# Kernel tuning notes

Hardware: AMD Instinct MI355X
Metric: run time of the kernel (lower is better)

## Reference

```python
import jax, jax.numpy as jnp
import numpy as np

N = 8192      # points
K = 16        # nsample neighbors
CIN = 64      # in_plane
C = 256       # out_plane (== mid_planes)
S = 8         # share_planes
EPS = 1e-5


def _bn(x, g, b, axes):
    # BatchNorm1d (training-mode batch stats, biased var), channel = last dim
    m = x.mean(axes, keepdims=True)
    v = x.var(axes, keepdims=True)
    return (x - m) / jnp.sqrt(v + EPS) * g + b


def _knn(p, k):
    # brute-force KNN over a single batch (o = [N]); indices include self
    sq = jnp.sum(p * p, axis=1)
    d2 = sq[:, None] + sq[None, :] - 2.0 * (p @ p.T)   # [N, N]
    idx = jax.lax.top_k(-d2, k)[1]                      # [N, K]
    return jax.lax.stop_gradient(idx)


def setup_inputs() -> dict:
    key = jax.random.key(0)
    ks = jax.random.split(key, 16)
    W = lambda i, shp, s=0.05: jax.random.normal(ks[i], shp, jnp.float32) * s
    one = lambda d: jnp.ones((d,), jnp.float32)
    zero = lambda d: jnp.zeros((d,), jnp.float32)
    return {
        "p": jax.random.normal(ks[0], (N, 3), jnp.float32),
        "x": jax.random.normal(ks[1], (N, CIN), jnp.float32),
        "o": jnp.array([N], dtype=jnp.int32),
        # PointAggregation (stride=1): Linear(no bias) + BN
        "W_pa": W(2, (CIN, C)), "g_pa": one(C), "b_pa": zero(C),
        # SelfFusion.linear1 (no bias) + bn1
        "W1": W(3, (C, C)), "g1": one(C), "b1": zero(C),
        # SelfFusionLayer q/k/v
        "Wq": W(4, (C, C)), "bq": zero(C),
        "Wk": W(5, (C, C)), "bk": zero(C),
        "Wv": W(6, (C, C)), "bv": zero(C),
        # linear_p: Linear(3,3)+BN(3)+ReLU+Linear(3,C)
        "Wp1": W(7, (3, 3), 0.3), "bp1": zero(3), "gp": one(3), "bp": zero(3),
        "Wp2": W(8, (3, C), 0.3), "bp2": zero(C),
        # linear_w: BN(C)+ReLU+Linear(C,C//S)+BN(C//S)+ReLU+Linear(C//S,C//S)
        "gw1": one(C), "bw1": zero(C),
        "Ww1": W(9, (C, C // S)), "bww1": zero(C // S),
        "gw2": one(C // S), "bw2": zero(C // S),
        "Ww2": W(10, (C // S, C // S), 0.2), "bww2": zero(C // S),
        # bn2, linear3 (no bias) + bn3
        "g2": one(C), "b2": zero(C),
        "W3": W(11, (C, C)), "g3": one(C), "b3": zero(C),
    }


def reference(p, x, o, W_pa, g_pa, b_pa, W1, g1, b1, Wq, bq, Wk, bk, Wv, bv,
              Wp1, bp1, gp, bp, Wp2, bp2, gw1, bw1, Ww1, bww1, gw2, bw2,
              Ww2, bww2, g2, b2, W3, g3, b3):
    relu = jax.nn.relu
    # --- PointAggregation (stride=1) ---
    h = relu(_bn(x @ W_pa, g_pa, b_pa, (0,)))          # [N, C]
    # --- SelfFusion block ---
    identity = h
    h = relu(_bn(h @ W1, g1, b1, (0,)))                # [N, C]
    # SelfFusionLayer
    xq = h @ Wq + bq                                   # [N, C]
    xk = h @ Wk + bk
    xv = h @ Wv + bv
    idx = _knn(p, K)                                   # [N, K]
    rel = p[idx] - p[:, None, :]                       # [N, K, 3] relative coords
    xk_g = xk[idx]                                     # [N, K, C]
    xv_g = xv[idx]                                     # [N, K, C]
    # linear_p: Linear(3,3) -> BN(3) -> ReLU -> Linear(3,C)
    p_r = rel @ Wp1 + bp1
    p_r = relu(_bn(p_r, gp, bp, (0, 1)))
    p_r = p_r @ Wp2 + bp2                              # [N, K, C]
    # mid_planes == out_planes so view(...).sum(2) is identity
    w = xk_g - xq[:, None, :] + p_r                    # [N, K, C]
    # linear_w: BN -> ReLU -> Linear -> BN -> ReLU -> Linear
    w = relu(_bn(w, gw1, bw1, (0, 1)))
    w = w @ Ww1 + bww1                                 # [N, K, C//S]
    w = relu(_bn(w, gw2, bw2, (0, 1)))
    w = w @ Ww2 + bww2                                 # [N, K, C//S]
    w = jax.nn.softmax(w, axis=1)                      # softmax over neighbors
    y = ((xv_g + p_r).reshape(N, K, S, C // S) * w[:, :, None, :]).sum(1)
    y = y.reshape(N, C)
    # back in SelfFusion
    y = relu(_bn(y, g2, b2, (0,)))
    y = _bn(y @ W3, g3, b3, (0,))
    x2 = relu(y + identity)
    return (p, x2, o)
```

## Files before the change

### kernel.cpp

```cpp
#include <hip/hip_runtime.h>
#include <hip/hip_bf16.h>

#define INV_N  (1.0f/8192.0f)
#define INV_NK (1.0f/131072.0f)

typedef __attribute__((ext_vector_type(8))) short bf16x8;
typedef __attribute__((ext_vector_type(4))) float f32x4;
typedef unsigned short u16;

__device__ __forceinline__ u16 f2b(float f) {
  unsigned u = __float_as_uint(f);
  return (u16)((u + 0x7FFFu + ((u >> 16) & 1u)) >> 16);
}
__device__ __forceinline__ float b2f(u16 u) {
  return __uint_as_float(((unsigned)u) << 16);
}

__device__ __forceinline__ float bn_ap(float v, const float* st, int C, int ch,
                                       float inv, float g, float b) {
  float m = st[ch] * inv;
  float var = st[C + ch] * inv - m * m;
  return (v - m) * rsqrtf(var + 1e-5f) * g + b;
}

__launch_bounds__(256)
__global__ void prep_k(const float* __restrict__ p, const int* __restrict__ o,
                       const float* __restrict__ Ww1,
                       float4* __restrict__ pp, u16* __restrict__ Ww1t,
                       float* __restrict__ st, float* __restrict__ out) {
  int b = blockIdx.x, t = threadIdx.x;
  int e = b*256 + t;
  if (b < 16) st[b*256 + t] = 0.f;
  if (e < 24576) out[e] = p[e];
  if (e == 0) out[24576 + 2097152] = (float)o[0];
  if (e < 8192) {
    float x = p[e*3+0], y = p[e*3+1], z = p[e*3+2];
    pp[e] = make_float4(x, y, z, (x*x + y*y) + z*z);
  }
  if (b >= 88) {
    int q = (b - 88)*1024 + t*4;
#pragma unroll
    for (int ii = 0; ii < 4; ++ii) {
      int e2 = q + ii;
      int k = e2 >> 5, n = e2 & 31;
      Ww1t[n*256 + k] = f2b(Ww1[e2]);
    }
  }
}

template<int ROWS, int SPLIT>
__launch_bounds__(256)
__global__ void red_k(const float* __restrict__ part, float* __restrict__ outp,
                      int width) {
  int ncg = width >> 6;
  int cg = blockIdx.x % ncg, sp = blockIdx.x / ncg;
  int lane = threadIdx.x & 63, chunk = threadIdx.x >> 6;
  int c = cg*64 + lane;
  constexpr int R  = ROWS / SPLIT;
  constexpr int RC = R / 4;
  float s = 0.f;
  int i0 = sp*R + chunk*RC;
#pragma unroll 4
  for (int i = i0; i < i0 + RC; ++i) s += part[(size_t)i*width + c];
  __shared__ float red[4][64];
  red[chunk][lane] = s;
  __syncthreads();
  if (threadIdx.x < 64) {
    float v = red[0][lane] + red[1][lane] + red[2][lane] + red[3][lane];
    if (SPLIT == 1) outp[c] = v;
    else atomicAdd(&outp[c], v);
  }
}

__device__ __forceinline__ void knn_dev(char* smem, const float4* __restrict__ pp,
                                        int* __restrict__ idxo, int kb) {
  float4* buf = (float4*)smem;
  int t = threadIdx.x;
  int wave = t >> 6, lane = t & 63;
  int q = kb*4 + wave;
  float4 qv = pp[q];
  const float BIG = __uint_as_float(0x7F7FFFFFu);
  float d[3];
#pragma unroll
  for (int s = 0; s < 3; ++s) d[s] = BIG;
  for (int ch = 0; ch < 8; ++ch) {
#pragma unroll
    for (int s = 0; s < 4; ++s)
      buf[s*256 + t] = pp[ch*1024 + s*256 + t];
    __syncthreads();
#pragma unroll 4
    for (int it = 0; it < 16; ++it) {
      int jl = it*64 + lane;
      float4 c = buf[jl];
      int j = ch*1024 + jl;
      float dot = qv.x*c.x + (qv.y*c.y + qv.z*c.z);
      float d2 = __fmaf_rn(-2.0f, dot, qv.w + c.w);
      float pk = __uint_as_float((__float_as_uint(d2) & 0xFFFFE000u) | (unsigned)j);
      d[2] = fminf(fmaxf(d[1], pk), d[2]);
      d[1] = fminf(fmaxf(d[0], pk), d[1]);
      d[0] = fminf(d[0], pk);
    }
    __syncthreads();
  }
  for (int r = 0; r < 16; ++r) {
    float bd = d[0];
#pragma unroll
    for (int m = 1; m < 64; m <<= 1)
      bd = fminf(bd, __shfl_xor(bd, m));
    if (lane == 0) idxo[q*16 + r] = (int)(__float_as_uint(bd) & 0x1FFFu);
    if (d[0] == bd) { d[0] = d[1]; d[1] = d[2]; d[2] = BIG; }
  }
}

template<typename TA, typename TO, bool BNA, bool STATS>
__device__ __forceinline__ void mfgemm_dev(char* smem,
    const TA* __restrict__ A, const float* __restrict__ st,
    const float* __restrict__ g, const float* __restrict__ bb, float inv_cnt,
    const float* __restrict__ W, TO* __restrict__ out,
    float* __restrict__ stout, int KA, int NOUT, int bm, int bn_) {
  short (*As)[72] = (short(*)[72])smem;
  short (*Bt)[72] = (short(*)[72])(smem + 9216);
  float* lscl = (float*)(smem + 18432);
  float* lsft = (float*)(smem + 19456);
  int t = threadIdx.x;
  int m0 = bm * 64, n0 = bn_ * 64;
  if (BNA) {
    for (int e = t; e < KA; e += 256) {
      float m = st[e] * inv_cnt;
      float var = st[KA + e] * inv_cnt - m*m;
      float sc = rsqrtf(var + 1e-5f) * g[e];
      lscl[e] = sc; lsft[e] = bb[e] - m*sc;
    }
    __syncthreads();
  }
  const f32x4 zero = {0.f, 0.f, 0.f, 0.f};
  f32x4 acc[2][2] = {{zero, zero}, {zero, zero}};
  int wv = t >> 6, l = t & 63;
  int wm = wv & 1, wn = wv >> 1;
  int lr = l & 15, lk = (l >> 4) * 8;
  int ra = t >> 4, qa = t & 15;
  int bn = t & 63, bkc = t >> 6;
  for (int k0 = 0; k0 < KA; k0 += 64) {
#pragma unroll
    for (int rp = 0; rp < 4; ++rp) {
      int r = rp*16 + ra;
      float vv[4];
      if constexpr (sizeof(TA) == 4) {
        float4 av = *(const float4*)((const float*)A + (size_t)(m0 + r)*KA + k0 + qa*4);
        vv[0] = av.x; vv[1] = av.y; vv[2] = av.z; vv[3] = av.w;
      } else {
        short4 av = *(const short4*)((const u16*)A + (size_t)(m0 + r)*KA + k0 + qa*4);
#pragma unroll
        for (int jj = 0; jj < 4; ++jj) vv[jj] = b2f(((u16*)&av)[jj]);
      }
      short4 s;
#pragma unroll
      for (int jj = 0; jj < 4; ++jj) {
        float v = vv[jj];
        if (BNA) { int ch = k0 + qa*4 + jj; v = fmaxf(fmaf(v, lscl[ch], lsft[ch]), 0.f); }
        ((u16*)&s)[jj] = f2b(v);
      }
      *(short4*)&As[r][qa*4] = s;
    }
    {
      float v[16];
#pragma unroll
      for (int j2 = 0; j2 < 16; ++j2)
        v[j2] = W[(size_t)(k0 + bkc*16 + j2)*NOUT + n0 + bn];
      bf16x8 w0, w1v;
#pragma unroll
      for (int j2 = 0; j2 < 8; ++j2) {
        w0[j2]  = (short)f2b(v[j2]);
        w1v[j2] = (short)f2b(v[8 + j2]);
      }
      *(bf16x8*)&Bt[bn][bkc*16]     = w0;
      *(bf16x8*)&Bt[bn][bkc*16 + 8] = w1v;
    }
    __syncthreads();
#pragma unroll
    for (int fk = 0; fk < 2; ++fk) {
      bf16x8 a0 = *(const bf16x8*)&As[wm*32 +      lr][fk*32 + lk];
      bf16x8 a1 = *(const bf16x8*)&As[wm*32 + 16 + lr][fk*32 + lk];
      bf16x8 b0 = *(const bf16x8*)&Bt[wn*32 +      lr][fk*32 + lk];
      bf16x8 b1 = *(const bf16x8*)&Bt[wn*32 + 16 + lr][fk*32 + lk];
      acc[0][0] = __builtin_amdgcn_mfma_f32_16x16x32_bf16(a0, b0, acc[0][0], 0, 0, 0);
      acc[0][1] = __builtin_amdgcn_mfma_f32_16x16x32_bf16(a0, b1, acc[0][1], 0, 0, 0);
      acc[1][0] = __builtin_amdgcn_mfma_f32_16x16x32_bf16(a1, b0, acc[1][0], 0, 0, 0);
      acc[1][1] = __builtin_amdgcn_mfma_f32_16x16x32_bf16(a1, b1, acc[1][1], 0, 0, 0);
    }
    __syncthreads();
  }
#pragma unroll
  for (int fn = 0; fn < 2; ++fn) {
    int col = n0 + wn*32 + fn*16 + lr;
    float s1 = 0.f, s2 = 0.f;
#pragma unroll
    for (int fm = 0; fm < 2; ++fm) {
#pragma unroll
      for (int r = 0; r < 4; ++r) {
        int row = m0 + wm*32 + fm*16 + (l >> 4)*4 + r;
        float v = acc[fm][fn][r];
        if constexpr (sizeof(TO) == 4) out[(size_t)row*NOUT + col] = v;
        else                           out[(size_t)row*NOUT + col] = f2b(v);
        if (STATS) { s1 += v; s2 += v*v; }
      }
    }
    if (STATS) {
      s1 += __shfl_xor(s1, 16); s1 += __shfl_xor(s1, 32);
      s2 += __shfl_xor(s2, 16); s2 += __shfl_xor(s2, 32);
      if (l < 16) {
        atomicAdd(&stout[col], s1);
        atomicAdd(&stout[NOUT + col], s2);
      }
    }
  }
}

__device__ __forceinline__ void comp_pr1(const float* p, int i, int j,
                                         const float* Wp1, const float* bp1,
                                         float pr1[3]) {
  float rx = p[j*3+0] - p[i*3+0];
  float ry = p[j*3+1] - p[i*3+1];
  float rz = p[j*3+2] - p[i*3+2];
#pragma unroll
  for (int c = 0; c < 3; ++c)
    pr1[c] = rx*Wp1[c] + ry*Wp1[3+c] + rz*Wp1[6+c] + bp1[c];
}

__device__ __forceinline__ void comp_prv(const float* p, int i, int j,
                                         const float* Wp1, const float* bp1,
                                         const float* gp, const float* bpp,
                                         const float* sp, float o3[3]) {
  float pr1[3];
  comp_pr1(p, i, j, Wp1, bp1, pr1);
#pragma unroll
  for (int c = 0; c < 3; ++c)
    o3[c] = fmaxf(bn_ap(pr1[c], sp, 3, c, INV_NK, gp[c], bpp[c]), 0.0f);
}

__device__ __forceinline__ void prstats_dev(char* smem,
    const float* __restrict__ p, const int* __restrict__ idx,
    const float* Wp1, const float* bp1, float* __restrict__ sp, int pb) {
  float s[3] = {0,0,0}, s2[3] = {0,0,0};
  for (int it = 0; it < 4; ++it) {
    int e = pb*1024 + it*256 + threadIdx.x;
    int i = e >> 4;
    int j = idx[e] & 8191;
    float pr1[3];
    comp_pr1(p, i, j, Wp1, bp1, pr1);
#pragma unroll
    for (int c = 0; c < 3; ++c) { s[c] += pr1[c]; s2[c] += pr1[c]*pr1[c]; }
  }
#pragma unroll
  for (int m = 1; m < 64; m <<= 1) {
#pragma unroll
    for (int c = 0; c < 3; ++c) {
      s[c]  += __shfl_xor(s[c],  m);
      s2[c] += __shfl_xor(s2[c], m);
    }
  }
  float (*red)[6] = (float(*)[6])smem;
  int wv = threadIdx.x >> 6, lane = threadIdx.x & 63;
  if (lane == 0) {
#pragma unroll
    for (int c = 0; c < 3; ++c) { red[wv][c] = s[c]; red[wv][3+c] = s2[c]; }
  }
  __syncthreads();
  if (threadIdx.x < 6) {
    float v = red[0][threadIdx.x] + red[1][threadIdx.x] +
              red[2][threadIdx.x] + red[3][threadIdx.x];
    atomicAdd(&sp[threadIdx.x], v);
  }
}

__launch_bounds__(256)
__global__ void gemmknn_k(const float* __restrict__ x, const float* __restrict__ W_pa,
                          u16* __restrict__ t0, float* __restrict__ st0,
                          const float4* __restrict__ pp, int* __restrict__ idxo) {
  extern __shared__ char smem[];
  int b = blockIdx.x;
  if (b < 512)
    mfgemm_dev<float, u16, false, true>(smem, x, nullptr, nullptr, nullptr, 0.f,
                                        W_pa, t0, st0, 64, 256, b & 127, b >> 7);
  else
    knn_dev(smem, pp, idxo, b - 512);
}

__launch_bounds__(256)
__global__ void gemmpr_k(const u16* __restrict__ t0, const float* __restrict__ st0,
                         const float* __restrict__ g_pa, const float* __restrict__ b_pa,
                         const float* __restrict__ W1, u16* __restrict__ t1,
                         float* __restrict__ st1,
                         const float* __restrict__ p, const int* __restrict__ idx,
                         const float* __restrict__ Wp1, const float* __restrict__ bp1,
                         float* __restrict__ sp) {
  extern __shared__ char smem[];
  int b = blockIdx.x;
  if (b < 512)
    mfgemm_dev<u16, u16, true, true>(smem, t0, st0, g_pa, b_pa, INV_N,
                                     W1, t1, st1, 256, 256, b & 127, b >> 7);
  else
    prstats_dev(smem, p, idx, Wp1, bp1, sp, b - 512);
}

template<typename TA, typename TO, bool BNA, bool STATS>
__launch_bounds__(256)
__global__ void mfgemm_k(const TA* __restrict__ A, const float* __restrict__ st,
                         const float* __restrict__ g, const float* __restrict__ bb,
                         float inv_cnt,
                         const float* __restrict__ W, TO* __restrict__ out,
                         float* __restrict__ stout, int KA, int NOUT) {
  extern __shared__ char smem[];
  mfgemm_dev<TA, TO, BNA, STATS>(smem, A, st, g, bb, inv_cnt, W, out, stout,
                                 KA, NOUT, blockIdx.x, blockIdx.y);
}

__launch_bounds__(256)
__global__ void qkv_k(const u16* __restrict__ t1, const float* __restrict__ st,
                      const float* __restrict__ g1, const float* __restrict__ b1,
                      const float* __restrict__ Wq, const float* __restrict__ bq,
                      const float* __restrict__ Wk, const float* __restrict__ bk,
                      const float* __restrict__ Wv, const float* __restrict__ bv,
                      u16* __restrict__ xq, u16* __restrict__ xk, u16* __restrict__ xv) {
  __shared__ short As[64][72];
  __shared__ short Bt[3][64][72];
  __shared__ float lscl[256], lsft[256];
  int t = threadIdx.x;
  int m0 = blockIdx.x * 64, n0 = blockIdx.y * 64;
  {
    int e = t;
    float m = st[e] * INV_N;
    float var = st[256 + e] * INV_N - m*m;
    float sc = rsqrtf(var + 1e-5f) * g1[e];
    lscl[e] = sc; lsft[e] = b1[e] - m*sc;
  }
  __syncthreads();
  const f32x4 zero = {0.f, 0.f, 0.f, 0.f};
  f32x4 acc[3][2][2];
#pragma unroll
  for (int w = 0; w < 3; ++w)
#pragma unroll
    for (int i = 0; i < 2; ++i)
#pragma unroll
      for (int j = 0; j < 2; ++j) acc[w][i][j] = zero;
  int wv = t >> 6, l = t & 63;
  int wm = wv & 1, wn = wv >> 1;
  int lr = l & 15, lk = (l >> 4) * 8;
  int ra = t >> 4, qa = t & 15;
  int bn = t & 63, bkc = t >> 6;
  const float* Ws[3] = {Wq, Wk, Wv};
  for (int k0 = 0; k0 < 256; k0 += 64) {
#pragma unroll
    for (int rp = 0; rp < 4; ++rp) {
      int r = rp*16 + ra;
      short4 av = *(const short4*)(t1 + (size_t)(m0 + r)*256 + k0 + qa*4);
      short4 s;
#pragma unroll
      for (int jj = 0; jj < 4; ++jj) {
        int ch = k0 + qa*4 + jj;
        float v = fmaxf(fmaf(b2f(((u16*)&av)[jj]), lscl[ch], lsft[ch]), 0.f);
        ((u16*)&s)[jj] = f2b(v);
      }
      *(short4*)&As[r][qa*4] = s;
    }
#pragma unroll
    for (int w = 0; w < 3; ++w) {
      float v[16];
#pragma unroll
      for (int j2 = 0; j2 < 16; ++j2)
        v[j2] = Ws[w][(size_t)(k0 + bkc*16 + j2)*256 + n0 + bn];
      bf16x8 w0, w1v;
#pragma unroll
      for (int j2 = 0; j2 < 8; ++j2) {
        w0[j2]  = (short)f2b(v[j2]);
        w1v[j2] = (short)f2b(v[8 + j2]);
      }
      *(bf16x8*)&Bt[w][bn][bkc*16]     = w0;
      *(bf16x8*)&Bt[w][bn][bkc*16 + 8] = w1v;
    }
    __syncthreads();
#pragma unroll
    for (int fk = 0; fk < 2; ++fk) {
      bf16x8 a0 = *(const bf16x8*)&As[wm*32 +      lr][fk*32 + lk];
      bf16x8 a1 = *(const bf16x8*)&As[wm*32 + 16 + lr][fk*32 + lk];
#pragma unroll
      for (int w = 0; w < 3; ++w) {
        bf16x8 b0 = *(const bf16x8*)&Bt[w][wn*32 +      lr][fk*32 + lk];
        bf16x8 b1 = *(const bf16x8*)&Bt[w][wn*32 + 16 + lr][fk*32 + lk];
        acc[w][0][0] = __builtin_amdgcn_mfma_f32_16x16x32_bf16(a0, b0, acc[w][0][0], 0, 0, 0);
        acc[w][0][1] = __builtin_amdgcn_mfma_f32_16x16x32_bf16(a0, b1, acc[w][0][1], 0, 0, 0);
        acc[w][1][0] = __builtin_amdgcn_mfma_f32_16x16x32_bf16(a1, b0, acc[w][1][0], 0, 0, 0);
        acc[w][1][1] = __builtin_amdgcn_mfma_f32_16x16x32_bf16(a1, b1, acc[w][1][1], 0, 0, 0);
      }
    }
    __syncthreads();
  }
  u16* outs[3] = {xq, xk, xv};
  const float* bs[3] = {bq, bk, bv};
#pragma unroll
  for (int w = 0; w < 3; ++w) {
#pragma unroll
    for (int fn = 0; fn < 2; ++fn) {
      int col = n0 + wn*32 + fn*16 + lr;
      float bvv = bs[w][col];
#pragma unroll
      for (int fm = 0; fm < 2; ++fm) {
#pragma unroll
        for (int r = 0; r < 4; ++r) {
          int row = m0 + wm*32 + fm*16 + (l >> 4)*4 + r;
          outs[w][(size_t)row*256 + col] = f2b(acc[w][fm][fn][r] + bvv);
        }
      }
    }
  }
}

__launch_bounds__(256)
__global__ void stats256_k(const u16* __restrict__ X, float* __restrict__ psy) {
  int c = threadIdx.x;
  int r0 = blockIdx.x * 32;
  float s1 = 0.f, s2 = 0.f;
  for (int r = 0; r < 32; ++r) {
    float v = b2f(X[(size_t)(r0 + r)*256 + c]);
    s1 += v; s2 += v*v;
  }
  psy[(size_t)blockIdx.x*512 + c]       = s1;
  psy[(size_t)blockIdx.x*512 + 256 + c] = s2;
}

__launch_bounds__(256)
__global__ void wstats_k(const u16* __restrict__ xk, const u16* __restrict__ xq,
                         const float* __restrict__ p, const int* __restrict__ idx,
                         const float* Wp1, const float* bp1, const float* gp, const float* bpp,
                         const float* sp, const float* __restrict__ Wp2, const float* bp2,
                         float* __restrict__ pws) {
  __shared__ float prv[8][16][4];
  __shared__ int   jidx[8][16];
  int base = blockIdx.x * 8;
  int t = threadIdx.x;
  if (t < 128) {
    int pt = t >> 4, k = t & 15;
    int j = idx[(base + pt)*16 + k] & 8191;
    jidx[pt][k] = j;
    float o3[3];
    comp_prv(p, base + pt, j, Wp1, bp1, gp, bpp, sp, o3);
    prv[pt][k][0] = o3[0]; prv[pt][k][1] = o3[1]; prv[pt][k][2] = o3[2];
  }
  __syncthreads();
  int c = t;
  float wp0 = Wp2[c], wp1v = Wp2[256+c], wp2v = Wp2[512+c];
  float bbv = bp2[c];
  float s1 = 0.f, s2 = 0.f;
  for (int pt = 0; pt < 8; ++pt) {
    int i = base + pt;
    float xqv = b2f(xq[(size_t)i*256 + c]);
    u16 kvals[16];
#pragma unroll
    for (int k = 0; k < 16; ++k)
      kvals[k] = xk[(size_t)jidx[pt][k]*256 + c];
#pragma unroll
    for (int k = 0; k < 16; ++k) {
      float pr = prv[pt][k][0]*wp0 + prv[pt][k][1]*wp1v + prv[pt][k][2]*wp2v + bbv;
      float wval = b2f(kvals[k]) - xqv + pr;
      s1 += wval; s2 += wval*wval;
    }
  }
  pws[(size_t)blockIdx.x*512 + c]       = s1;
  pws[(size_t)blockIdx.x*512 + 256 + c] = s2;
}

__launch_bounds__(256)
__global__ void w1gemm_k(const u16* __restrict__ xk, const u16* __restrict__ xq,
                         const float* __restrict__ p, const int* __restrict__ idx,
                         const float* Wp1, const float* bp1, const float* gp, const float* bpp,
                         const float* sp, const float* __restrict__ Wp2, const float* bp2,
                         const float* sw, const float* gw1, const float* bw1,
                         const u16* __restrict__ Ww1t, const float* bww1,
                         u16* __restrict__ w1, float* __restrict__ pw1) {
  __shared__ short sA[64][264];
  __shared__ float prv[64][3];
  __shared__ int   jrow[64];
  __shared__ float sred[256];
  int t = threadIdx.x;
  int base4 = blockIdx.x * 4;
  if (t < 64) {
    int grow = blockIdx.x*64 + t;
    int j = idx[grow] & 8191;
    jrow[t] = j;
    float o3[3];
    comp_prv(p, grow >> 4, j, Wp1, bp1, gp, bpp, sp, o3);
    prv[t][0] = o3[0]; prv[t][1] = o3[1]; prv[t][2] = o3[2];
  }
  __syncthreads();
  {
    int o = t & 31, rs = t >> 5;
    int ch0 = o*8;
    int jr[8];
#pragma unroll
    for (int ii = 0; ii < 8; ++ii) jr[ii] = jrow[ii*8 + rs];
    bf16x8 kvv[8], qvv[8];
#pragma unroll
    for (int ii = 0; ii < 8; ++ii) {
      int r = ii*8 + rs;
      kvv[ii] = *(const bf16x8*)(xk + (size_t)jr[ii]*256 + ch0);
      qvv[ii] = *(const bf16x8*)(xq + (size_t)(base4 + (r >> 4))*256 + ch0);
    }
    float sclv[8], sftv[8], w0v[8], w1vv[8], w2v[8], b2v[8];
#pragma unroll
    for (int h = 0; h < 2; ++h) {
      float4 swm = *(const float4*)(sw + ch0 + h*4);
      float4 sws = *(const float4*)(sw + 256 + ch0 + h*4);
      float4 g4  = *(const float4*)(gw1 + ch0 + h*4);
      float4 bb4 = *(const float4*)(bw1 + ch0 + h*4);
      float4 p0v = *(const float4*)(Wp2 + ch0 + h*4);
      float4 p1v = *(const float4*)(Wp2 + 256 + ch0 + h*4);
      float4 p2v = *(const float4*)(Wp2 + 512 + ch0 + h*4);
      float4 bp4 = *(const float4*)(bp2 + ch0 + h*4);
      float mv[4] = {swm.x, swm.y, swm.z, swm.w};
      float sv[4] = {sws.x, sws.y, sws.z, sws.w};
      float gv[4] = {g4.x, g4.y, g4.z, g4.w};
      float bv[4] = {bb4.x, bb4.y, bb4.z, bb4.w};
      float a0[4] = {p0v.x, p0v.y, p0v.z, p0v.w};
      float a1[4] = {p1v.x, p1v.y, p1v.z, p1v.w};
      float a2[4] = {p2v.x, p2v.y, p2v.z, p2v.w};
      float a3[4] = {bp4.x, bp4.y, bp4.z, bp4.w};
#pragma unroll
      for (int jj = 0; jj < 4; ++jj) {
        int e = h*4 + jj;
        float m = mv[jj]*INV_NK;
        float var = sv[jj]*INV_NK - m*m;
        float sc = rsqrtf(var + 1e-5f)*gv[jj];
        sclv[e] = sc; sftv[e] = bv[jj] - m*sc;
        w0v[e] = a0[jj]; w1vv[e] = a1[jj]; w2v[e] = a2[jj]; b2v[e] = a3[jj];
      }
    }
#pragma unroll
    for (int ii = 0; ii < 8; ++ii) {
      int r = ii*8 + rs;
      float p0 = prv[r][0], p1 = prv[r][1], p2 = prv[r][2];
      bf16x8 av;
#pragma unroll
      for (int e = 0; e < 8; ++e) {
        float v = b2f((u16)kvv[ii][e]) - b2f((u16)qvv[ii][e])
                + p0*w0v[e] + p1*w1vv[e] + p2*w2v[e] + b2v[e];
        v = fmaxf(fmaf(v, sclv[e], sftv[e]), 0.f);
        av[e] = (short)f2b(v);
      }
      *(bf16x8*)&sA[r][ch0] = av;
    }
  }
  __syncthreads();
  const f32x4 zero = {0.f,0.f,0.f,0.f};
  f32x4 acc[2] = {zero, zero};
  int wv = t >> 6, l = t & 63;
  int lr = l & 15, hi = l >> 4;
#pragma unroll
  for (int k0 = 0; k0 < 8; ++k0) {
    int kb = k0*32 + hi*8;
    bf16x8 a  = *(const bf16x8*)&sA[wv*16 + lr][kb];
    bf16x8 b0 = *(const bf16x8*)(Ww1t + (size_t)lr*256      + kb);
    bf16x8 b1 = *(const bf16x8*)(Ww1t + (size_t)(16+lr)*256 + kb);
    acc[0] = __builtin_amdgcn_mfma_f32_16x16x32_bf16(a, b0, acc[0], 0, 0, 0);
    acc[1] = __builtin_amdgcn_mfma_f32_16x16x32_bf16(a, b1, acc[1], 0, 0, 0);
  }
#pragma unroll
  for (int fn = 0; fn < 2; ++fn) {
    int col = fn*16 + lr;
    float bv = bww1[col];
    float s1 = 0.f, s2 = 0.f;
#pragma unroll
    for (int r = 0; r < 4; ++r) {
      int grow = blockIdx.x*64 + wv*16 + hi*4 + r;
      float v = acc[fn][r] + bv;
      w1[(size_t)grow*32 + col] = f2b(v);
      s1 += v; s2 += v*v;
    }
    s1 += __shfl_xor(s1, 16); s1 += __shfl_xor(s1, 32);
    s2 += __shfl_xor(s2, 16); s2 += __shfl_xor(s2, 32);
    if (l < 16) { sred[(wv*2+fn)*16 + lr] = s1; sred[128 + (wv*2+fn)*16 + lr] = s2; }
  }
  __syncthreads();
  if (t < 32) {
    float a = 0.f, b = 0.f;
#pragma unroll
    for (int w2 = 0; w2 < 4; ++w2) {
      a += sred[(w2*2 + (t >> 4))*16 + (t & 15)];
      b += sred[128 + (w2*2 + (t >> 4))*16 + (t & 15)];
    }
    pw1[(size_t)blockIdx.x*64 + t]      = a;
    pw1[(size_t)blockIdx.x*64 + 32 + t] = b;
  }
}

__launch_bounds__(256)
__global__ void aggr_k(const u16* __restrict__ w1, const float* sw1,
                       const float* gw2, const float* bw2,
                       const float* __restrict__ Ww2, const float* bww2,
                       const u16* __restrict__ xv,
                       const float* __restrict__ p, const int* __restrict__ idx,
                       const float* Wp1, const float* bp1, const float* gp, const float* bpp,
                       const float* sp, const float* __restrict__ Wp2, const float* bp2,
                       u16* __restrict__ y) {
  __shared__ float lw1[16][32];
  __shared__ float lW2[32][32];
  __shared__ float sw2[16][33];
  __shared__ float prv[16][4];
  __shared__ int   jidx[16];
  int i = blockIdx.x, t = threadIdx.x;
  for (int e = t; e < 1024; e += 256) lW2[e >> 5][e & 31] = Ww2[e];
  for (int e = t; e < 512; e += 256) {
    int c32 = e & 31;
    float v = b2f(w1[(size_t)i*512 + e]);
    v = fmaxf(bn_ap(v, sw1, 32, c32, INV_NK, gw2[c32], bw2[c32]), 0.0f);
    lw1[e >> 5][c32] = v;
  }
  if (t < 16) jidx[t] = idx[i*16 + t] & 8191;
  __syncthreads();
  if (t < 16) {
    float o3[3];
    comp_prv(p, i, jidx[t], Wp1, bp1, gp, bpp, sp, o3);
    prv[t][0] = o3[0]; prv[t][1] = o3[1]; prv[t][2] = o3[2];
  }
  for (int e = t; e < 512; e += 256) {
    int k = e >> 5, c32 = e & 31;
    float a = bww2[c32];
#pragma unroll
    for (int j = 0; j < 32; ++j) a += lw1[k][j] * lW2[j][c32];
    sw2[k][c32] = a;
  }
  __syncthreads();
  if (t < 32) {
    float mx = -3.0e38f;
#pragma unroll
    for (int k = 0; k < 16; ++k) mx = fmaxf(mx, sw2[k][t]);
    float s = 0.f;
#pragma unroll
    for (int k = 0; k < 16; ++k) { float e2 = expf(sw2[k][t] - mx); sw2[k][t] = e2; s += e2; }
    float r = 1.0f / s;
#pragma unroll
    for (int k = 0; k < 16; ++k) sw2[k][t] *= r;
  }
  __syncthreads();
  int c = t;
  float wp0 = Wp2[c], wp1v = Wp2[256+c], wp2v = Wp2[512+c];
  float bbv = bp2[c];
  int c32 = c & 31;
  float acc = 0.f;
#pragma unroll
  for (int k = 0; k < 16; ++k) {
    int j = jidx[k];
    float pr = prv[k][0]*wp0 + prv[k][1]*wp1v + prv[k][2]*wp2v + bbv;
    float xvv = b2f(xv[(size_t)j*256 + c]);
    acc += (xvv + pr) * sw2[k][c32];
  }
  y[(size_t)i*256 + c] = f2b(acc);
}

__launch_bounds__(256)
__global__ void final_k(const u16* __restrict__ t0, const float* s0,
                        const float* g0, const float* b0,
                        const u16* __restrict__ t3, const float* s3,
                        const float* g3, const float* b3,
                        float* __restrict__ out) {
  int i = blockIdx.x, c = threadIdx.x;
  size_t off = (size_t)i*256 + c;
  float h0 = fmaxf(bn_ap(b2f(t0[off]), s0, 256, c, INV_N, g0[c], b0[c]), 0.0f);
  float v3 = bn_ap(b2f(t3[off]), s3, 256, c, INV_N, g3[c], b3[c]);
  out[24576 + off] = fmaxf(v3 + h0, 0.0f);
}

extern "C" void kernel_launch(void* const* d_in, const int* in_sizes, int n_in,
                              void* d_out, int out_size, void* d_ws, size_t ws_size,
                              hipStream_t stream) {
  (void)in_sizes; (void)n_in; (void)out_size; (void)ws_size;
  const float* p    = (const float*)d_in[0];
  const float* x    = (const float*)d_in[1];
  const int*   o    = (const int*)  d_in[2];
  const float* W_pa = (const float*)d_in[3];
  const float* g_pa = (const float*)d_in[4];
  const float* b_pa = (const float*)d_in[5];
  const float* W1   = (const float*)d_in[6];
  const float* g1   = (const float*)d_in[7];
  const float* b1   = (const float*)d_in[8];
  const float* Wq   = (const float*)d_in[9];
  const float* bq   = (const float*)d_in[10];
  const float* Wk   = (const float*)d_in[11];
  const float* bk   = (const float*)d_in[12];
  const float* Wv   = (const float*)d_in[13];
  const float* bv   = (const float*)d_in[14];
  const float* Wp1  = (const float*)d_in[15];
  const float* bp1  = (const float*)d_in[16];
  const float* gp   = (const float*)d_in[17];
  const float* bpp  = (const float*)d_in[18];
  const float* Wp2  = (const float*)d_in[19];
  const float* bp2  = (const float*)d_in[20];
  const float* gw1  = (const float*)d_in[21];
  const float* bw1  = (const float*)d_in[22];
  const float* Ww1  = (const float*)d_in[23];
  const float* bww1 = (const float*)d_in[24];
  const float* gw2  = (const float*)d_in[25];
  const float* bw2  = (const float*)d_in[26];
  const float* Ww2  = (const float*)d_in[27];
  const float* bww2 = (const float*)d_in[28];
  const float* g2   = (const float*)d_in[29];
  const float* b2   = (const float*)d_in[30];
  const float* W3   = (const float*)d_in[31];
  const float* g3   = (const float*)d_in[32];
  const float* b3   = (const float*)d_in[33];

  char* ws = (char*)d_ws;
  u16*   t0  = (u16*)  (ws + 0);
  u16*   t1  = (u16*)  (ws + 4194304);
  u16*   xq  = (u16*)  (ws + 8388608);
  u16*   xk  = (u16*)  (ws + 12582912);
  u16*   xv  = (u16*)  (ws + 16777216);
  u16*   w1  = (u16*)  (ws + 20971520);
  int*   idx = (int*)  (ws + 29360128);
  float* st  = (float*)(ws + 29884416);
  u16*   Ww1t= (u16*)  (ws + 29900800);
  float* pw1 = (float*)(ws + 30408704);
  float* pws = (float*)(ws + 30932992);
  float* psy = (float*)(ws + 33030144);
  u16*   y   = t1;
  u16*   t3  = xq;
  float4* pp = (float4*)(ws + 20971520);

  prep_k<<<96, 256, 0, stream>>>(p, o, Ww1, pp, Ww1t, st, (float*)d_out);

  gemmknn_k<<<2560, 256, 20480, stream>>>(x, W_pa, t0, st + 0, pp, idx);

  gemmpr_k<<<640, 256, 20480, stream>>>(t0, st + 0, g_pa, b_pa, W1, t1, st + 512,
                                        p, idx, Wp1, bp1, st + 2624);

  qkv_k<<<dim3(128, 4), 256, 0, stream>>>(
      t1, st + 512, g1, b1, Wq, bq, Wk, bk, Wv, bv, xq, xk, xv);

  wstats_k<<<1024, 256, 0, stream>>>(xk, xq, p, idx, Wp1, bp1, gp, bpp,
                                     st + 2624, Wp2, bp2, pws);
  red_k<1024, 4><<<32, 256, 0, stream>>>(pws, st + 1024, 512);

  w1gemm_k<<<2048, 256, 0, stream>>>(xk, xq, p, idx, Wp1, bp1, gp, bpp,
                                     st + 2624, Wp2, bp2, st + 1024,
                                     gw1, bw1, Ww1t, bww1, w1, pw1);
  red_k<2048, 16><<<16, 256, 0, stream>>>(pw1, st + 2560, 64);

  aggr_k<<<8192, 256, 0, stream>>>(w1, st + 2560, gw2, bw2, Ww2, bww2, xv,
                                   p, idx, Wp1, bp1, gp, bpp, st + 2624,
                                   Wp2, bp2, y);
  stats256_k<<<256, 256, 0, stream>>>(y, psy);
  red_k<256, 2><<<16, 256, 0, stream>>>(psy, st + 1536, 512);

  mfgemm_k<u16, u16, true, true><<<dim3(128, 4), 256, 20480, stream>>>(
      y, st + 1536, g2, b2, INV_N, W3, t3, st + 2048, 256, 256);

  final_k<<<8192, 256, 0, stream>>>(t0, st + 0, g_pa, b_pa,
                                    t3, st + 2048, g3, b3, (float*)d_out);
}
```

Before: 187.2 us.

## Spread KNN blocks across the GEMM and QKV launches to overlap work

The KNN search used to share one launch with the first small GEMM. It is now split into two halves: one half runs alongside the second GEMM and the other alongside the QKV projection, each launched as extra blocks. The first GEMM becomes a standalone launch, and the pr-stats reduction moves into its own kernel after idx is complete. The aim is to balance the heterogeneous work across launches so the KNN fills idle compute units during the heavier GEMMs. In exchange it adds one kernel launch, and the QKV kernel now uses dynamic shared memory sized for its tiles (38912 B).

```diff
diff --git a/kernel.cpp b/kernel.cpp
--- a/kernel.cpp
+++ b/kernel.cpp
@@ -238,12 +238,12 @@
     o3[c] = fmaxf(bn_ap(pr1[c], sp, 3, c, INV_NK, gp[c], bpp[c]), 0.0f);
 }
 
-__device__ __forceinline__ void prstats_dev(char* smem,
-    const float* __restrict__ p, const int* __restrict__ idx,
-    const float* Wp1, const float* bp1, float* __restrict__ sp, int pb) {
+__launch_bounds__(256)
+__global__ void prstats_k(const float* __restrict__ p, const int* __restrict__ idx,
+                          const float* Wp1, const float* bp1, float* __restrict__ sp) {
   float s[3] = {0,0,0}, s2[3] = {0,0,0};
   for (int it = 0; it < 4; ++it) {
-    int e = pb*1024 + it*256 + threadIdx.x;
+    int e = blockIdx.x*1024 + it*256 + threadIdx.x;
     int i = e >> 4;
     int j = idx[e] & 8191;
     float pr1[3];
@@ -259,7 +259,7 @@
       s2[c] += __shfl_xor(s2[c], m);
     }
   }
-  float (*red)[6] = (float(*)[6])smem;
+  __shared__ float red[4][6];
   int wv = threadIdx.x >> 6, lane = threadIdx.x & 63;
   if (lane == 0) {
 #pragma unroll
@@ -273,34 +273,106 @@
   }
 }
 
-__launch_bounds__(256)
-__global__ void gemmknn_k(const float* __restrict__ x, const float* __restrict__ W_pa,
-                          u16* __restrict__ t0, float* __restrict__ st0,
-                          const float4* __restrict__ pp, int* __restrict__ idxo) {
-  extern __shared__ char smem[];
-  int b = blockIdx.x;
-  if (b < 512)
-    mfgemm_dev<float, u16, false, true>(smem, x, nullptr, nullptr, nullptr, 0.f,
-                                        W_pa, t0, st0, 64, 256, b & 127, b >> 7);
-  else
-    knn_dev(smem, pp, idxo, b - 512);
-}
-
-__launch_bounds__(256)
-__global__ void gemmpr_k(const u16* __restrict__ t0, const float* __restrict__ st0,
-                         const float* __restrict__ g_pa, const float* __restrict__ b_pa,
-                         const float* __restrict__ W1, u16* __restrict__ t1,
-                         float* __restrict__ st1,
-                         const float* __restrict__ p, const int* __restrict__ idx,
-                         const float* __restrict__ Wp1, const float* __restrict__ bp1,
-                         float* __restrict__ sp) {
-  extern __shared__ char smem[];
-  int b = blockIdx.x;
-  if (b < 512)
-    mfgemm_dev<u16, u16, true, true>(smem, t0, st0, g_pa, b_pa, INV_N,
-                                     W1, t1, st1, 256, 256, b & 127, b >> 7);
-  else
-    prstats_dev(smem, p, idx, Wp1, bp1, sp, b - 512);
+__device__ __forceinline__ void qkv_dev(char* smem,
+    const u16* __restrict__ t1, const float* __restrict__ st,
+    const float* __restrict__ g1, const float* __restrict__ b1,
+    const float* __restrict__ Wq, const float* __restrict__ bq,
+    const float* __restrict__ Wk, const float* __restrict__ bk,
+    const float* __restrict__ Wv, const float* __restrict__ bv,
+    u16* __restrict__ xq, u16* __restrict__ xk, u16* __restrict__ xv_,
+    int bm, int bn_) {
+  short (*As)[72] = (short(*)[72])smem;
+  short (*Bt)[64][72] = (short(*)[64][72])(smem + 9216);
+  float* lscl = (float*)(smem + 36864);
+  float* lsft = (float*)(smem + 37888);
+  int t = threadIdx.x;
+  int m0 = bm * 64, n0 = bn_ * 64;
+  {
+    int e = t;
+    float m = st[e] * INV_N;
+    float var = st[256 + e] * INV_N - m*m;
+    float sc = rsqrtf(var + 1e-5f) * g1[e];
+    lscl[e] = sc; lsft[e] = b1[e] - m*sc;
+  }
+  __syncthreads();
+  const f32x4 zero = {0.f, 0.f, 0.f, 0.f};
+  f32x4 acc[3][2][2];
+#pragma unroll
+  for (int w = 0; w < 3; ++w)
+#pragma unroll
+    for (int i = 0; i < 2; ++i)
+#pragma unroll
+      for (int j = 0; j < 2; ++j) acc[w][i][j] = zero;
+  int wv = t >> 6, l = t & 63;
+  int wm = wv & 1, wn = wv >> 1;
+  int lr = l & 15, lk = (l >> 4) * 8;
+  int ra = t >> 4, qa = t & 15;
+  int bn = t & 63, bkc = t >> 6;
+  const float* Ws[3] = {Wq, Wk, Wv};
+  for (int k0 = 0; k0 < 256; k0 += 64) {
+#pragma unroll
+    for (int rp = 0; rp < 4; ++rp) {
+      int r = rp*16 + ra;
+      short4 av = *(const short4*)(t1 + (size_t)(m0 + r)*256 + k0 + qa*4);
+      short4 s;
+#pragma unroll
+      for (int jj = 0; jj < 4; ++jj) {
+        int ch = k0 + qa*4 + jj;
+        float v = fmaxf(fmaf(b2f(((u16*)&av)[jj]), lscl[ch], lsft[ch]), 0.f);
+        ((u16*)&s)[jj] = f2b(v);
+      }
+      *(short4*)&As[r][qa*4] = s;
+    }
+#pragma unroll
+    for (int w = 0; w < 3; ++w) {
+      float v[16];
+#pragma unroll
+      for (int j2 = 0; j2 < 16; ++j2)
+        v[j2] = Ws[w][(size_t)(k0 + bkc*16 + j2)*256 + n0 + bn];
+      bf16x8 w0, w1v;
+#pragma unroll
+      for (int j2 = 0; j2 < 8; ++j2) {
+        w0[j2]  = (short)f2b(v[j2]);
+        w1v[j2] = (short)f2b(v[8 + j2]);
+      }
+      *(bf16x8*)&Bt[w][bn][bkc*16]     = w0;
+      *(bf16x8*)&Bt[w][bn][bkc*16 + 8] = w1v;
+    }
+    __syncthreads();
+#pragma unroll
+    for (int fk = 0; fk < 2; ++fk) {
+      bf16x8 a0 = *(const bf16x8*)&As[wm*32 +      lr][fk*32 + lk];
+      bf16x8 a1 = *(const bf16x8*)&As[wm*32 + 16 + lr][fk*32 + lk];
+#pragma unroll
+      for (int w = 0; w < 3; ++w) {
+        bf16x8 b0 = *(const bf16x8*)&Bt[w][wn*32 +      lr][fk*32 + lk];
+        bf16x8 b1 = *(const bf16x8*)&Bt[w][wn*32 + 16 + lr][fk*32 + lk];
+        acc[w][0][0] = __builtin_amdgcn_mfma_f32_16x16x32_bf16(a0, b0, acc[w][0][0], 0, 0, 0);
+        acc[w][0][1] = __builtin_amdgcn_mfma_f32_16x16x32_bf16(a0, b1, acc[w][0][1], 0, 0, 0);
+        acc[w][1][0] = __builtin_amdgcn_mfma_f32_16x16x32_bf16(a1, b0, acc[w][1][0], 0, 0, 0);
+        acc[w][1][1] = __builtin_amdgcn_mfma_f32_16x16x32_bf16(a1, b1, acc[w][1][1], 0, 0, 0);
+      }
+    }
+    __syncthreads();
+  }
+  u16* outs[3] = {xq, xk, xv_};
+  const float* bs[3] = {bq, bk, bv};
+#pragma unroll
+  for (int w = 0; w < 3; ++w) {
+#pragma unroll
+    for (int fn = 0; fn < 2; ++fn) {
+      int col = n0 + wn*32 + fn*16 + lr;
+      float bvv = bs[w][col];
+#pragma unroll
+      for (int fm = 0; fm < 2; ++fm) {
+#pragma unroll
+        for (int r = 0; r < 4; ++r) {
+          int row = m0 + wm*32 + fm*16 + (l >> 4)*4 + r;
+          outs[w][(size_t)row*256 + col] = f2b(acc[w][fm][fn][r] + bvv);
+        }
+      }
+    }
+  }
 }
 
 template<typename TA, typename TO, bool BNA, bool STATS>
@@ -316,103 +388,35 @@
 }
 
 __launch_bounds__(256)
-__global__ void qkv_k(const u16* __restrict__ t1, const float* __restrict__ st,
-                      const float* __restrict__ g1, const float* __restrict__ b1,
-                      const float* __restrict__ Wq, const float* __restrict__ bq,
-                      const float* __restrict__ Wk, const float* __restrict__ bk,
-                      const float* __restrict__ Wv, const float* __restrict__ bv,
-                      u16* __restrict__ xq, u16* __restrict__ xk, u16* __restrict__ xv) {
-  __shared__ short As[64][72];
-  __shared__ short Bt[3][64][72];
-  __shared__ float lscl[256], lsft[256];
-  int t = threadIdx.x;
-  int m0 = blockIdx.x * 64, n0 = blockIdx.y * 64;
-  {
-    int e = t;
-    float m = st[e] * INV_N;
-    float var = st[256 + e] * INV_N - m*m;
-    float sc = rsqrtf(var + 1e-5f) * g1[e];
-    lscl[e] = sc; lsft[e] = b1[e] - m*sc;
-  }
-  __syncthreads();
-  const f32x4 zero = {0.f, 0.f, 0.f, 0.f};
-  f32x4 acc[3][2][2];
-#pragma unroll
-  for (int w = 0; w < 3; ++w)
-#pragma unroll
-    for (int i = 0; i < 2; ++i)
-#pragma unroll
-      for (int j = 0; j < 2; ++j) acc[w][i][j] = zero;
-  int wv = t >> 6, l = t & 63;
-  int wm = wv & 1, wn = wv >> 1;
-  int lr = l & 15, lk = (l >> 4) * 8;
-  int ra = t >> 4, qa = t & 15;
-  int bn = t & 63, bkc = t >> 6;
-  const float* Ws[3] = {Wq, Wk, Wv};
-  for (int k0 = 0; k0 < 256; k0 += 64) {
-#pragma unroll
-    for (int rp = 0; rp < 4; ++rp) {
-      int r = rp*16 + ra;
-      short4 av = *(const short4*)(t1 + (size_t)(m0 + r)*256 + k0 + qa*4);
-      short4 s;
-#pragma unroll
-      for (int jj = 0; jj < 4; ++jj) {
-        int ch = k0 + qa*4 + jj;
-        float v = fmaxf(fmaf(b2f(((u16*)&av)[jj]), lscl[ch], lsft[ch]), 0.f);
-        ((u16*)&s)[jj] = f2b(v);
-      }
-      *(short4*)&As[r][qa*4] = s;
-    }
-#pragma unroll
-    for (int w = 0; w < 3; ++w) {
-      float v[16];
-#pragma unroll
-      for (int j2 = 0; j2 < 16; ++j2)
-        v[j2] = Ws[w][(size_t)(k0 + bkc*16 + j2)*256 + n0 + bn];
-      bf16x8 w0, w1v;
-#pragma unroll
-      for (int j2 = 0; j2 < 8; ++j2) {
-        w0[j2]  = (short)f2b(v[j2]);
-        w1v[j2] = (short)f2b(v[8 + j2]);
-      }
-      *(bf16x8*)&Bt[w][bn][bkc*16]     = w0;
-      *(bf16x8*)&Bt[w][bn][bkc*16 + 8] = w1v;
-    }
-    __syncthreads();
-#pragma unroll
-    for (int fk = 0; fk < 2; ++fk) {
-      bf16x8 a0 = *(const bf16x8*)&As[wm*32 +      lr][fk*32 + lk];
-      bf16x8 a1 = *(const bf16x8*)&As[wm*32 + 16 + lr][fk*32 + lk];
-#pragma unroll
-      for (int w = 0; w < 3; ++w) {
-        bf16x8 b0 = *(const bf16x8*)&Bt[w][wn*32 +      lr][fk*32 + lk];
-        bf16x8 b1 = *(const bf16x8*)&Bt[w][wn*32 + 16 + lr][fk*32 + lk];
-        acc[w][0][0] = __builtin_amdgcn_mfma_f32_16x16x32_bf16(a0, b0, acc[w][0][0], 0, 0, 0);
-        acc[w][0][1] = __builtin_amdgcn_mfma_f32_16x16x32_bf16(a0, b1, acc[w][0][1], 0, 0, 0);
-        acc[w][1][0] = __builtin_amdgcn_mfma_f32_16x16x32_bf16(a1, b0, acc[w][1][0], 0, 0, 0);
-        acc[w][1][1] = __builtin_amdgcn_mfma_f32_16x16x32_bf16(a1, b1, acc[w][1][1], 0, 0, 0);
-      }
-    }
-    __syncthreads();
-  }
-  u16* outs[3] = {xq, xk, xv};
-  const float* bs[3] = {bq, bk, bv};
-#pragma unroll
-  for (int w = 0; w < 3; ++w) {
-#pragma unroll
-    for (int fn = 0; fn < 2; ++fn) {
-      int col = n0 + wn*32 + fn*16 + lr;
-      float bvv = bs[w][col];
-#pragma unroll
-      for (int fm = 0; fm < 2; ++fm) {
-#pragma unroll
-        for (int r = 0; r < 4; ++r) {
-          int row = m0 + wm*32 + fm*16 + (l >> 4)*4 + r;
-          outs[w][(size_t)row*256 + col] = f2b(acc[w][fm][fn][r] + bvv);
-        }
-      }
-    }
-  }
+__global__ void gemm2knn_k(const u16* __restrict__ t0, const float* __restrict__ st0,
+                           const float* __restrict__ g_pa, const float* __restrict__ b_pa,
+                           const float* __restrict__ W1, u16* __restrict__ t1,
+                           float* __restrict__ st1,
+                           const float4* __restrict__ pp, int* __restrict__ idxo) {
+  extern __shared__ char smem[];
+  int b = blockIdx.x;
+  if (b < 512)
+    mfgemm_dev<u16, u16, true, true>(smem, t0, st0, g_pa, b_pa, INV_N,
+                                     W1, t1, st1, 256, 256, b & 127, b >> 7);
+  else
+    knn_dev(smem, pp, idxo, b - 512);
+}
+
+__launch_bounds__(256)
+__global__ void qkvknn_k(const u16* __restrict__ t1, const float* __restrict__ st1,
+                         const float* __restrict__ g1, const float* __restrict__ b1,
+                         const float* __restrict__ Wq, const float* __restrict__ bq,
+                         const float* __restrict__ Wk, const float* __restrict__ bk,
+                         const float* __restrict__ Wv, const float* __restrict__ bv,
+                         u16* __restrict__ xq, u16* __restrict__ xk, u16* __restrict__ xv,
+                         const float4* __restrict__ pp, int* __restrict__ idxo) {
+  extern __shared__ char smem[];
+  int b = blockIdx.x;
+  if (b < 512)
+    qkv_dev(smem, t1, st1, g1, b1, Wq, bq, Wk, bk, Wv, bv, xq, xk, xv,
+            b & 127, b >> 7);
+  else
+    knn_dev(smem, pp, idxo, 512 + b);
 }
 
 __launch_bounds__(256)
@@ -727,13 +731,16 @@
 
   prep_k<<<96, 256, 0, stream>>>(p, o, Ww1, pp, Ww1t, st, (float*)d_out);
 
-  gemmknn_k<<<2560, 256, 20480, stream>>>(x, W_pa, t0, st + 0, pp, idx);
-
-  gemmpr_k<<<640, 256, 20480, stream>>>(t0, st + 0, g_pa, b_pa, W1, t1, st + 512,
-                                        p, idx, Wp1, bp1, st + 2624);
-
-  qkv_k<<<dim3(128, 4), 256, 0, stream>>>(
-      t1, st + 512, g1, b1, Wq, bq, Wk, bk, Wv, bv, xq, xk, xv);
+  mfgemm_k<float, u16, false, true><<<dim3(128, 4), 256, 20480, stream>>>(
+      x, nullptr, nullptr, nullptr, 0.f, W_pa, t0, st + 0, 64, 256);
+
+  gemm2knn_k<<<1536, 256, 20480, stream>>>(t0, st + 0, g_pa, b_pa, W1, t1,
+                                           st + 512, pp, idx);
+
+  qkvknn_k<<<1536, 256, 38912, stream>>>(t1, st + 512, g1, b1, Wq, bq, Wk, bk,
+                                         Wv, bv, xq, xk, xv, pp, idx);
+
+  prstats_k<<<128, 256, 0, stream>>>(p, idx, Wp1, bp1, st + 2624);
 
   wstats_k<<<1024, 256, 0, stream>>>(xk, xq, p, idx, Wp1, bp1, gp, bpp,
                                      st + 2624, Wp2, bp2, pws);
```

After: 206.5 us. 1.1x slower.
